# Performance work log

Measured on AMD Instinct MI355X. Metric: run time of the kernel, lower is better.

## Reference

```python
import jax, jax.numpy as jnp
import numpy as np

SIGMA = 5.0
THRESH = 0.1

def setup_inputs() -> dict:
    key = jax.random.key(0)
    k1, k2, k3 = jax.random.split(key, 3)
    B, N, H, W = 8, 20, 512, 512
    y_pred = jax.random.normal(k1, (B, 1, H, W), dtype=jnp.float32)
    point_labels = jax.random.randint(k2, (B, N), 0, 2, dtype=jnp.int32)
    point_coords = jax.random.uniform(k3, (B, N, 2), dtype=jnp.float32)
    return {"y_pred": y_pred, "point_labels": point_labels, "point_coords": point_coords}


def _soft_labels(point_labels, point_coords, H, W):
    # Replicates the sequential overwrite-scatter: for each pixel, the LAST
    B, N = point_labels.shape
    yc = point_coords[..., 0] * H  # (B, N)
    xc = point_coords[..., 1] * W  # (B, N)
    yg = jnp.arange(H, dtype=jnp.float32)
    xg = jnp.arange(W, dtype=jnp.float32)
    # (B, N, H, W) squared distance from each point to each pixel
    dist_sq = (yg[None, None, :, None] - yc[:, :, None, None]) ** 2 \
            + (xg[None, None, None, :] - xc[:, :, None, None]) ** 2
    mask = jnp.exp(-dist_sq / (2.0 * SIGMA ** 2)) > THRESH  # (B, N, H, W)
    n_idx = jnp.arange(N, dtype=jnp.int32)[None, :, None, None]
    last = jnp.max(jnp.where(mask, n_idx, -1), axis=1)  # (B, H, W); -1 = no point
    valid = last >= 0
    labels = jnp.take_along_axis(
        point_labels.astype(jnp.float32)[:, :, None], last.clip(0).reshape(B, 1, -1)[:, 0][:, None, :].swapaxes(1, 2)[..., 0][:, None, :], axis=1
    ) if False else point_labels.astype(jnp.float32)[jnp.arange(B)[:, None, None], last.clip(0)]
    return labels, valid


def reference(y_pred, point_labels, point_coords):
    B, _, H, W = y_pred.shape
    labels, valid = _soft_labels(point_labels, point_coords, H, W)
    logits = y_pred[:, 0]  # (B, H, W)
    # numerically-stable BCE with logits
    bce = jnp.maximum(logits, 0.0) - logits * labels + jnp.log1p(jnp.exp(-jnp.abs(logits)))
    cnt = valid.sum()
    loss = jnp.where(cnt > 0,
                     jnp.sum(bce * valid) / jnp.maximum(cnt, 1).astype(jnp.float32),
                     jnp.float32(0.0))
    return loss
```

## Files before the change

kernel.cpp:

```cpp
#include <hip/hip_runtime.h>
#include <math.h>


#define R2_THRESH 115.12925464970229f
#define HW 512
#define NPTS 20
#define NBLOCKS 512
#define MAGIC 0x5F3C9A17u
#define MAGIC2 0x5F3C9A175F3C9A17ull

__global__ __launch_bounds__(256)
void pce_kernel(const float* __restrict__ y_pred,
                const int* __restrict__ point_labels,
                const float* __restrict__ point_coords,
                unsigned long long* __restrict__ slots,
                unsigned* __restrict__ flags,
                float* __restrict__ out) {
    const int bid  = blockIdx.x;
    const int b    = bid >> 6;
    const int y0   = (bid & 63) * 8;
    const int tid  = threadIdx.x;
    const int r    = tid >> 5;
    const int lane = tid & 31;

    __shared__ float s_strip[8][HW];
    __shared__ float s_xc[8][NPTS], s_lim[8][NPTS], s_lab[8][NPTS];

    const float4* grow = (const float4*)(y_pred + (size_t)b * HW * HW + (size_t)(y0 + r) * HW);
    float4 v0 = grow[lane];
    float4 v1 = grow[lane + 32];
    float4 v2 = grow[lane + 64];
    float4 v3 = grow[lane + 96];

    float xlo = INFINITY, xhi = -INFINITY;
    if (lane < NPTS) {
        float2 cc = ((const float2*)point_coords)[b * NPTS + lane];
        float yc  = cc.x * (float)HW;
        float xc  = cc.y * (float)HW;
        float dy  = (float)(y0 + r) - yc;
        float lim = R2_THRESH - dy * dy;
        s_xc[r][lane]  = xc;
        s_lim[r][lane] = lim;
        s_lab[r][lane] = (float)point_labels[b * NPTS + lane];
        if (lim > 0.0f) {
            float s = sqrtf(lim);
            xlo = xc - s;
            xhi = xc + s;
        }
    }
    #pragma unroll
    for (int off = 16; off > 0; off >>= 1) {
        xlo = fminf(xlo, __shfl_xor(xlo, off, 32));
        xhi = fmaxf(xhi, __shfl_xor(xhi, off, 32));
    }
    const int x0 = (int)fminf(fmaxf(floorf(xlo), 0.0f), 512.0f);
    const int x1 = (int)fminf(fmaxf(ceilf(xhi), -1.0f), 511.0f);

    {
        float4* dst = (float4*)&s_strip[r][0];
        dst[lane]      = v0;
        dst[lane + 32] = v1;
        dst[lane + 64] = v2;
        dst[lane + 96] = v3;
    }
    __syncthreads();

    float sum = 0.0f, cnt = 0.0f;
    for (int px = x0 + lane; px <= x1; px += 32) {
        float l = s_strip[r][px];
        const float fx = (float)px;
        float lab = 0.0f;
        bool  valid = false;
        #pragma unroll
        for (int k = 0; k < NPTS; ++k) {
            float dx = fx - s_xc[r][k];
            if (dx * dx < s_lim[r][k]) { lab = s_lab[r][k]; valid = true; }
        }
        if (valid) {
            sum += fmaxf(l, 0.0f) - l * lab + log1pf(expf(-fabsf(l)));
            cnt += 1.0f;
        }
    }

    #pragma unroll
    for (int off = 32; off > 0; off >>= 1) {
        sum += __shfl_down(sum, off, 64);
        cnt += __shfl_down(cnt, off, 64);
    }
    __shared__ float rs[4], rc[4];
    if ((tid & 63) == 0) { rs[tid >> 6] = sum; rc[tid >> 6] = cnt; }
    __syncthreads();
    if (tid == 0) {
        float S = rs[0] + rs[1] + rs[2] + rs[3];
        float C = rc[0] + rc[1] + rc[2] + rc[3];
        unsigned long long w = ((unsigned long long)__float_as_uint(C) << 32)
                             | (unsigned long long)__float_as_uint(S);
        __hip_atomic_store(&slots[bid], w, __ATOMIC_RELAXED, __HIP_MEMORY_SCOPE_AGENT);
        __hip_atomic_store(&flags[bid], MAGIC, __ATOMIC_RELEASE, __HIP_MEMORY_SCOPE_AGENT);
    }
    if (bid != 0) return;

    {
        unsigned long long f = 0;
        unsigned long long* fp = (unsigned long long*)&flags[2 * tid];
        do {
            f = __hip_atomic_load(fp, __ATOMIC_ACQUIRE, __HIP_MEMORY_SCOPE_AGENT);
            if (f != MAGIC2) __builtin_amdgcn_s_sleep(1);
        } while (f != MAGIC2);
    }

    {
        unsigned long long w0 = __hip_atomic_load(&slots[2 * tid + 0], __ATOMIC_RELAXED, __HIP_MEMORY_SCOPE_AGENT);
        unsigned long long w1 = __hip_atomic_load(&slots[2 * tid + 1], __ATOMIC_RELAXED, __HIP_MEMORY_SCOPE_AGENT);
        float S = __uint_as_float((unsigned)(w0 & 0xffffffffull))
                + __uint_as_float((unsigned)(w1 & 0xffffffffull));
        float C = __uint_as_float((unsigned)(w0 >> 32))
                + __uint_as_float((unsigned)(w1 >> 32));
        #pragma unroll
        for (int off = 32; off > 0; off >>= 1) {
            S += __shfl_down(S, off, 64);
            C += __shfl_down(C, off, 64);
        }
        if ((tid & 63) == 0) { rs[tid >> 6] = S; rc[tid >> 6] = C; }
        __syncthreads();
        if (tid == 0) {
            float SS = rs[0] + rs[1] + rs[2] + rs[3];
            float CC = rc[0] + rc[1] + rc[2] + rc[3];
            out[0] = (CC > 0.0f) ? (SS / CC) : 0.0f;
        }
        __hip_atomic_store(&flags[2 * tid + 0], 0u, __ATOMIC_RELAXED, __HIP_MEMORY_SCOPE_AGENT);
        __hip_atomic_store(&flags[2 * tid + 1], 0u, __ATOMIC_RELAXED, __HIP_MEMORY_SCOPE_AGENT);
    }
}

extern "C" void kernel_launch(void* const* d_in, const int* in_sizes, int n_in,
                              void* d_out, int out_size, void* d_ws, size_t ws_size,
                              hipStream_t stream) {
    const float* y_pred       = (const float*)d_in[0];
    const int*   point_labels = (const int*)d_in[1];
    const float* point_coords = (const float*)d_in[2];
    float*       out          = (float*)d_out;

    char* w = (char*)d_ws;
    unsigned long long* slots = (unsigned long long*)(w);
    unsigned*           flags = (unsigned*)(w + 4096);

    pce_kernel<<<NBLOCKS, 256, 0, stream>>>(y_pred, point_labels, point_coords,
                                            slots, flags, out);
}
```

Before: 19.62 us.

## Let any block that observes all flags finalize, single-wave reduction

Every block's first wave now checks all 512 completion flags once and, if every one is set, computes and writes the final loss itself. Block 0 still spins until all flags are set, then finalizes and clears them. The final reduction is done by one 64-lane wave with 8 slots per lane, which removes the shared-memory step and the block barrier. The aim is to shorten the tail where block 0 waits for late blocks, at the cost of extra flag reads by every block and possibly several redundant writes of the same result.

```diff
diff --git a/kernel.cpp b/kernel.cpp
--- a/kernel.cpp
+++ b/kernel.cpp
@@ -8,6 +8,24 @@
 #define NBLOCKS 512
 #define MAGIC 0x5F3C9A17u
 #define MAGIC2 0x5F3C9A175F3C9A17ull
+
+__device__ __forceinline__ void finalize64(const unsigned long long* slots,
+                                           float* out, int t) {
+    float S = 0.0f, C = 0.0f;
+    #pragma unroll
+    for (int j = 0; j < 8; ++j) {
+        unsigned long long w = __hip_atomic_load(&slots[8 * t + j],
+                                                 __ATOMIC_RELAXED, __HIP_MEMORY_SCOPE_AGENT);
+        S += __uint_as_float((unsigned)(w & 0xffffffffull));
+        C += __uint_as_float((unsigned)(w >> 32));
+    }
+    #pragma unroll
+    for (int off = 32; off > 0; off >>= 1) {
+        S += __shfl_down(S, off, 64);
+        C += __shfl_down(C, off, 64);
+    }
+    if (t == 0) out[0] = (C > 0.0f) ? (S / C) : 0.0f;
+}
 
 __global__ __launch_bounds__(256)
 void pce_kernel(const float* __restrict__ y_pred,
@@ -98,39 +116,38 @@
         __hip_atomic_store(&slots[bid], w, __ATOMIC_RELAXED, __HIP_MEMORY_SCOPE_AGENT);
         __hip_atomic_store(&flags[bid], MAGIC, __ATOMIC_RELEASE, __HIP_MEMORY_SCOPE_AGENT);
     }
-    if (bid != 0) return;
+    if (tid >= 64) return;
 
-    {
-        unsigned long long f = 0;
-        unsigned long long* fp = (unsigned long long*)&flags[2 * tid];
-        do {
-            f = __hip_atomic_load(fp, __ATOMIC_ACQUIRE, __HIP_MEMORY_SCOPE_AGENT);
-            if (f != MAGIC2) __builtin_amdgcn_s_sleep(1);
-        } while (f != MAGIC2);
+    const unsigned long long* fq = (const unsigned long long*)flags;
+
+    if (bid != 0) {
+        unsigned long long a0 = __hip_atomic_load(&fq[4 * tid + 0], __ATOMIC_ACQUIRE, __HIP_MEMORY_SCOPE_AGENT);
+        unsigned long long a1 = __hip_atomic_load(&fq[4 * tid + 1], __ATOMIC_ACQUIRE, __HIP_MEMORY_SCOPE_AGENT);
+        unsigned long long a2 = __hip_atomic_load(&fq[4 * tid + 2], __ATOMIC_ACQUIRE, __HIP_MEMORY_SCOPE_AGENT);
+        unsigned long long a3 = __hip_atomic_load(&fq[4 * tid + 3], __ATOMIC_ACQUIRE, __HIP_MEMORY_SCOPE_AGENT);
+        int ok = (a0 == MAGIC2) && (a1 == MAGIC2) && (a2 == MAGIC2) && (a3 == MAGIC2);
+        if (!__all(ok)) return;
+        finalize64(slots, out, tid);
+        return;
     }
 
     {
-        unsigned long long w0 = __hip_atomic_load(&slots[2 * tid + 0], __ATOMIC_RELAXED, __HIP_MEMORY_SCOPE_AGENT);
-        unsigned long long w1 = __hip_atomic_load(&slots[2 * tid + 1], __ATOMIC_RELAXED, __HIP_MEMORY_SCOPE_AGENT);
-        float S = __uint_as_float((unsigned)(w0 & 0xffffffffull))
-                + __uint_as_float((unsigned)(w1 & 0xffffffffull));
-        float C = __uint_as_float((unsigned)(w0 >> 32))
-                + __uint_as_float((unsigned)(w1 >> 32));
-        #pragma unroll
-        for (int off = 32; off > 0; off >>= 1) {
-            S += __shfl_down(S, off, 64);
-            C += __shfl_down(C, off, 64);
+        unsigned long long a0 = 0, a1 = 0, a2 = 0, a3 = 0;
+        for (;;) {
+            if (a0 != MAGIC2) a0 = __hip_atomic_load(&fq[4 * tid + 0], __ATOMIC_ACQUIRE, __HIP_MEMORY_SCOPE_AGENT);
+            if (a1 != MAGIC2) a1 = __hip_atomic_load(&fq[4 * tid + 1], __ATOMIC_ACQUIRE, __HIP_MEMORY_SCOPE_AGENT);
+            if (a2 != MAGIC2) a2 = __hip_atomic_load(&fq[4 * tid + 2], __ATOMIC_ACQUIRE, __HIP_MEMORY_SCOPE_AGENT);
+            if (a3 != MAGIC2) a3 = __hip_atomic_load(&fq[4 * tid + 3], __ATOMIC_ACQUIRE, __HIP_MEMORY_SCOPE_AGENT);
+            if (a0 == MAGIC2 && a1 == MAGIC2 && a2 == MAGIC2 && a3 == MAGIC2) break;
+            __builtin_amdgcn_s_sleep(1);
         }
-        if ((tid & 63) == 0) { rs[tid >> 6] = S; rc[tid >> 6] = C; }
-        __syncthreads();
-        if (tid == 0) {
-            float SS = rs[0] + rs[1] + rs[2] + rs[3];
-            float CC = rc[0] + rc[1] + rc[2] + rc[3];
-            out[0] = (CC > 0.0f) ? (SS / CC) : 0.0f;
-        }
-        __hip_atomic_store(&flags[2 * tid + 0], 0u, __ATOMIC_RELAXED, __HIP_MEMORY_SCOPE_AGENT);
-        __hip_atomic_store(&flags[2 * tid + 1], 0u, __ATOMIC_RELAXED, __HIP_MEMORY_SCOPE_AGENT);
     }
+    finalize64(slots, out, tid);
+    unsigned long long* fw = (unsigned long long*)flags;
+    __hip_atomic_store(&fw[4 * tid + 0], 0ull, __ATOMIC_RELAXED, __HIP_MEMORY_SCOPE_AGENT);
+    __hip_atomic_store(&fw[4 * tid + 1], 0ull, __ATOMIC_RELAXED, __HIP_MEMORY_SCOPE_AGENT);
+    __hip_atomic_store(&fw[4 * tid + 2], 0ull, __ATOMIC_RELAXED, __HIP_MEMORY_SCOPE_AGENT);
+    __hip_atomic_store(&fw[4 * tid + 3], 0ull, __ATOMIC_RELAXED, __HIP_MEMORY_SCOPE_AGENT);
 }
 
 extern "C" void kernel_launch(void* const* d_in, const int* in_sizes, int n_in,
```

Result: slower. 33.78 us (+72.2%).
